# Kernel optimization log

Measured on AMD Instinct MI355X. Metric: run time of the kernel, lower is better.

Reference implementation:

```python
import jax, jax.numpy as jnp
import numpy as np

H = 256   # encoder/decoder hidden size
U = 128   # attention units


def setup_inputs() -> dict:
    key = jax.random.key(0)
    ks = jax.random.split(key, 8)
    B, Td, Te = 16, 128, 1024
    s = 1.0 / np.sqrt(H)
    return {
        "dec_outputs": jax.random.normal(ks[0], (B, Td, H), dtype=jnp.float32),
        "enc_outputs": jax.random.normal(ks[1], (B, Te, H), dtype=jnp.float32),
        "W1": jax.random.normal(ks[2], (H, U), dtype=jnp.float32) * s,
        "b1": jnp.zeros((U,), dtype=jnp.float32),
        "W2": jax.random.normal(ks[3], (H, U), dtype=jnp.float32) * s,
        "b2": jnp.zeros((U,), dtype=jnp.float32),
        "V": jax.random.normal(ks[4], (U, 1), dtype=jnp.float32) * (1.0 / np.sqrt(U)),
        "bv": jnp.zeros((1,), dtype=jnp.float32),
    }


def reference(dec_outputs, enc_outputs, W1, b1, W2, b2, V, bv):
    # Project once (the original redundantly re-projects enc_outputs per step).
    # w1d: [B, Td, U], w2e: [B, Te, U]
    w1d = jnp.einsum("bth,hu->btu", dec_outputs, W1) + b1
    w2e = jnp.einsum("bsh,hu->bsu", enc_outputs, W2) + b2
    # Additive Bahdanau score: tanh over broadcast sum -> [B, Td, Te, U]
    feat = jnp.tanh(w1d[:, :, None, :] + w2e[:, None, :, :])
    # V projection to scalar score: [B, Td, Te]
    score = jnp.einsum("btsu,u->bts", feat, V[:, 0]) + bv[0]
    # Softmax over encoder positions (original Softmax(axis=1) on [B, Te])
    return jax.nn.softmax(score, axis=-1)
```

## Files before the change

kernel.cpp:

```cpp
#include <hip/hip_runtime.h>
#include <math.h>

#define HB 256
#define UB 128
#define BB 16
#define TD 128
#define TE 1024

#define CLAMP_W 7.0f
#define L2E2 2.8853900817779268f
#define ALPHA 1.52587890625e-05f
#define NEG2ALPHA (-3.0517578125e-05f)

__device__ __forceinline__ float stage_exp(float w, float shift) {
    float t = fminf(fmaxf(w, -CLAMP_W), CLAMP_W);
    return exp2f(fmaf(t, L2E2, shift));
}

#define DEC_SLABS 32
#define NSLABS 288
#define PROJ_BLOCKS (NSLABS * 2)

__global__ __launch_bounds__(512) void proj_v12(
    const float* __restrict__ dec, const float* __restrict__ enc,
    const float* __restrict__ W1, const float* __restrict__ b1,
    const float* __restrict__ W2, const float* __restrict__ b2,
    float* __restrict__ Ea, float* __restrict__ Eb) {
    const int blk = blockIdx.x;
    const int slab = blk >> 1, uhalf = blk & 1;
    const bool is_dec = slab < DEC_SLABS;
    const int rel = is_dec ? slab : slab - DEC_SLABS;
    const float* __restrict__ X    = is_dec ? dec : enc;
    const float* __restrict__ W    = is_dec ? W1 : W2;
    const float* __restrict__ bias = is_dec ? b1 : b2;

    __shared__ float xt[HB][66];
    const int tid = threadIdx.x;
    const long row0 = (long)rel * 64;

    #pragma unroll
    for (int it = 0; it < 8; ++it) {
        int idx = it * 512 + tid;
        int row = idx >> 6, hf4 = idx & 63;
        float4 f = *reinterpret_cast<const float4*>(X + (row0 + row) * HB + hf4 * 4);
        xt[hf4 * 4 + 0][row] = f.x;
        xt[hf4 * 4 + 1][row] = f.y;
        xt[hf4 * 4 + 2][row] = f.z;
        xt[hf4 * 4 + 3][row] = f.w;
    }
    __syncthreads();

    const int l = tid & 63;
    const int w = __builtin_amdgcn_readfirstlane(tid >> 6);
    const int ub3 = w & 3;
    const int ub  = ub3 + uhalf * 4;
    const int hh  = w >> 2;
    const int u0  = ub * 16;
    const int h0  = hh * 128;

    float acc[16];
    #pragma unroll
    for (int j = 0; j < 16; ++j) acc[j] = 0.f;

    for (int h = 0; h < 128; h += 4) {
        const int hg = h0 + h;
        float4 wf[4][4];
        #pragma unroll
        for (int k = 0; k < 4; ++k)
            #pragma unroll
            for (int q = 0; q < 4; ++q)
                wf[k][q] = *reinterpret_cast<const float4*>(
                    W + (hg + k) * UB + u0 + q * 4);
        float xk[4];
        #pragma unroll
        for (int k = 0; k < 4; ++k) xk[k] = xt[hg + k][l];
        #pragma unroll
        for (int k = 0; k < 4; ++k)
            #pragma unroll
            for (int q = 0; q < 4; ++q) {
                acc[q * 4 + 0] = fmaf(xk[k], wf[k][q].x, acc[q * 4 + 0]);
                acc[q * 4 + 1] = fmaf(xk[k], wf[k][q].y, acc[q * 4 + 1]);
                acc[q * 4 + 2] = fmaf(xk[k], wf[k][q].z, acc[q * 4 + 2]);
                acc[q * 4 + 3] = fmaf(xk[k], wf[k][q].w, acc[q * 4 + 3]);
            }
    }

    __syncthreads();
    float4* red = reinterpret_cast<float4*>(&xt[0][0]);
    if (hh == 1) {
        #pragma unroll
        for (int q = 0; q < 4; ++q)
            red[((ub3 * 64 + l) << 2) + q] =
                make_float4(acc[q * 4], acc[q * 4 + 1], acc[q * 4 + 2], acc[q * 4 + 3]);
    }
    __syncthreads();
    if (hh == 0) {
        #pragma unroll
        for (int q = 0; q < 4; ++q) {
            float4 r = red[((ub3 * 64 + l) << 2) + q];
            acc[q * 4 + 0] += r.x; acc[q * 4 + 1] += r.y;
            acc[q * 4 + 2] += r.z; acc[q * 4 + 3] += r.w;
        }
        const float sh = is_dec ? -16.f : 0.f;
        const int POS  = is_dec ? TD : TE;
        const long bq  = row0 / POS;
        const int pos  = (int)(row0 % POS) + l;
        float4* dst4 = reinterpret_cast<float4*>(is_dec ? Ea : Eb);
        #pragma unroll
        for (int q = 0; q < 4; ++q) {
            float4 o = make_float4(
                stage_exp(acc[q * 4 + 0] + bias[u0 + q * 4 + 0], sh),
                stage_exp(acc[q * 4 + 1] + bias[u0 + q * 4 + 1], sh),
                stage_exp(acc[q * 4 + 2] + bias[u0 + q * 4 + 2], sh),
                stage_exp(acc[q * 4 + 3] + bias[u0 + q * 4 + 3], sh));
            dst4[(bq * 32 + ub * 4 + q) * (long)POS + pos] = o;
        }
    }
}

__global__ __launch_bounds__(512) void score_v12(
    const float4* __restrict__ Ea4,
    const float4* __restrict__ Eb4,
    const float4* __restrict__ V4,
    float* __restrict__ outraw) {
    const int tid = threadIdx.x;
    const int i = blockIdx.x;
    const int xcd = i & 7;
    const int rest = i >> 3;
    const int b = 2 * xcd + (rest >> 6);
    const int sub = rest & 63;
    const int t0 = (sub >> 3) * 16;
    const int schunk = sub & 7;

    __shared__ float4 as[512];
    __shared__ float4 vs[32];
    as[tid] = Ea4[((long)b * 32 + (tid >> 4)) * TD + t0 + (tid & 15)];
    if (tid < 32) vs[tid] = V4[tid];
    __syncthreads();

    const int l = tid & 63, wv = tid >> 6;
    const int t = l & 15, sc = l >> 4;
    const int s0 = schunk * 128 + wv * 16 + sc * 4;

    const float4* __restrict__ ep = Eb4 + (long)b * 32 * TE + s0;
    const float alphav = ALPHA;
    float acc[4] = {0.f, 0.f, 0.f, 0.f};

    #pragma unroll 2
    for (int u4 = 0; u4 < 32; ++u4) {
        float4 A  = as[u4 * 16 + t];
        float4 v4 = vs[u4];
        #pragma unroll
        for (int j = 0; j < 4; ++j) {
            float4 e = ep[(long)u4 * TE + j];
            float X0 = fmaf(A.x, e.x, alphav);
            float X1 = fmaf(A.y, e.y, alphav);
            float X2 = fmaf(A.z, e.z, alphav);
            float X3 = fmaf(A.w, e.w, alphav);
            float P01 = X0 * X1, P23 = X2 * X3;
            float N01 = fmaf(v4.x, X1, v4.y * X0);
            float N23 = fmaf(v4.z, X3, v4.w * X2);
            float N   = fmaf(N01, P23, N23 * P01);
            acc[j] = fmaf(N, __builtin_amdgcn_rcpf(P01 * P23), acc[j]);
        }
    }

    float4 o = make_float4(NEG2ALPHA * acc[0], NEG2ALPHA * acc[1],
                           NEG2ALPHA * acc[2], NEG2ALPHA * acc[3]);
    *reinterpret_cast<float4*>(&outraw[((long)b * TD + t0 + t) * TE + s0]) = o;
}

__global__ __launch_bounds__(1024) void softmax_v9(float* __restrict__ out) {
    const long row = blockIdx.x;
    float* p = out + row * TE;
    const int tid = threadIdx.x;
    const int wv = tid >> 6, l = tid & 63;

    float x = p[tid];
    __shared__ float red[16];
    float m = x;
    #pragma unroll
    for (int off = 32; off > 0; off >>= 1) m = fmaxf(m, __shfl_xor(m, off, 64));
    if (l == 0) red[wv] = m;
    __syncthreads();
    #pragma unroll
    for (int k = 0; k < 16; ++k) m = fmaxf(m, red[k]);
    __syncthreads();
    float e = __expf(x - m);
    float si = e;
    #pragma unroll
    for (int off = 32; off > 0; off >>= 1) si += __shfl_xor(si, off, 64);
    if (l == 0) red[wv] = si;
    __syncthreads();
    si = 0.f;
    #pragma unroll
    for (int k = 0; k < 16; ++k) si += red[k];
    p[tid] = e * (1.f / si);
}

extern "C" void kernel_launch(void* const* d_in, const int* in_sizes, int n_in,
                              void* d_out, int out_size, void* d_ws, size_t ws_size,
                              hipStream_t stream) {
    const float* dec = (const float*)d_in[0];
    const float* enc = (const float*)d_in[1];
    const float* W1  = (const float*)d_in[2];
    const float* b1  = (const float*)d_in[3];
    const float* W2  = (const float*)d_in[4];
    const float* b2  = (const float*)d_in[5];
    const float* V   = (const float*)d_in[6];
    float* out = (float*)d_out;

    float* Ea = (float*)d_ws;
    float* Eb = Ea + (long)BB * 32 * TD * 4;

    proj_v12<<<PROJ_BLOCKS, 512, 0, stream>>>(dec, enc, W1, b1, W2, b2, Ea, Eb);
    score_v12<<<1024, 512, 0, stream>>>(
        (const float4*)Ea, (const float4*)Eb, (const float4*)V, out);
    softmax_v9<<<BB * TD, 1024, 0, stream>>>(out);
}
```

Before: 76.83 us.

## Rework score kernel to per-thread s column with scalar-loaded decoder tiles

New measurement: 67.86 us. -11.7%, faster.

```diff
diff --git a/kernel.cpp b/kernel.cpp
--- a/kernel.cpp
+++ b/kernel.cpp
@@ -11,6 +11,11 @@
 #define L2E2 2.8853900817779268f
 #define ALPHA 1.52587890625e-05f
 #define NEG2ALPHA (-3.0517578125e-05f)
+
+#define PINV(x) asm volatile("" : "+v"(x))
+#define PINS(x) asm volatile("" : "+s"(x))
+#define PINV4(q) do { PINV((q).x); PINV((q).y); PINV((q).z); PINV((q).w); } while (0)
+#define PINS4(q) do { PINS((q).x); PINS((q).y); PINS((q).z); PINS((q).w); } while (0)
 
 __device__ __forceinline__ float stage_exp(float w, float shift) {
     float t = fminf(fmaxf(w, -CLAMP_W), CLAMP_W);
@@ -118,56 +123,63 @@
     }
 }
 
-__global__ __launch_bounds__(512) void score_v12(
-    const float4* __restrict__ Ea4,
+__global__ __launch_bounds__(512) void score_v9(
+    const float* __restrict__ Ea4,
     const float4* __restrict__ Eb4,
-    const float4* __restrict__ V4,
+    const float* __restrict__ V,
     float* __restrict__ outraw) {
     const int tid = threadIdx.x;
     const int i = blockIdx.x;
-    const int xcd = i & 7;
-    const int rest = i >> 3;
-    const int b = 2 * xcd + (rest >> 6);
-    const int sub = rest & 63;
-    const int t0 = (sub >> 3) * 16;
-    const int schunk = sub & 7;
-
-    __shared__ float4 as[512];
-    __shared__ float4 vs[32];
-    as[tid] = Ea4[((long)b * 32 + (tid >> 4)) * TD + t0 + (tid & 15)];
-    if (tid < 32) vs[tid] = V4[tid];
-    __syncthreads();
-
-    const int l = tid & 63, wv = tid >> 6;
-    const int t = l & 15, sc = l >> 4;
-    const int s0 = schunk * 128 + wv * 16 + sc * 4;
-
-    const float4* __restrict__ ep = Eb4 + (long)b * 32 * TE + s0;
+    const int xcd = i & 7, j = i >> 3;
+    const int b     = 2 * xcd + (j >> 4);
+    const int tgrp  = (j >> 1) & 7;
+    const int shalf = j & 1;
+    const int t0 = tgrp * 16;
+    const int s  = shalf * 512 + tid;
+
+    const float*  ab = Ea4 + ((long)b * 32 * TD + t0) * 4;
+    const float4* ep = Eb4 + (long)b * 32 * TE + s;
     const float alphav = ALPHA;
-    float acc[4] = {0.f, 0.f, 0.f, 0.f};
-
-    #pragma unroll 2
+
+    float acc[16];
+    #pragma unroll
+    for (int t = 0; t < 16; ++t) acc[t] = 0.f;
+
+    float4 a[16], vC, vN, eC, eN;
+    vC = *reinterpret_cast<const float4*>(V);
+    eC = ep[0];
+
     for (int u4 = 0; u4 < 32; ++u4) {
-        float4 A  = as[u4 * 16 + t];
-        float4 v4 = vs[u4];
-        #pragma unroll
-        for (int j = 0; j < 4; ++j) {
-            float4 e = ep[(long)u4 * TE + j];
-            float X0 = fmaf(A.x, e.x, alphav);
-            float X1 = fmaf(A.y, e.y, alphav);
-            float X2 = fmaf(A.z, e.z, alphav);
-            float X3 = fmaf(A.w, e.w, alphav);
+        const int p = (u4 + 1 < 32) ? u4 + 1 : 0;
+        eN = ep[(long)p * TE];
+        vN = *reinterpret_cast<const float4*>(V + p * 4);
+        const float* _a = ab + (long)u4 * (TD * 4);
+        #pragma unroll
+        for (int t = 0; t < 16; ++t)
+            a[t] = *reinterpret_cast<const float4*>(_a + t * 4);
+        PINS4(a[15]);
+        #pragma unroll
+        for (int t = 0; t < 16; ++t) {
+            float4 A = a[t];
+            float X0 = fmaf(A.x, eC.x, alphav);
+            float X1 = fmaf(A.y, eC.y, alphav);
+            float X2 = fmaf(A.z, eC.z, alphav);
+            float X3 = fmaf(A.w, eC.w, alphav);
             float P01 = X0 * X1, P23 = X2 * X3;
-            float N01 = fmaf(v4.x, X1, v4.y * X0);
-            float N23 = fmaf(v4.z, X3, v4.w * X2);
+            float N01 = fmaf(vC.x, X1, vC.y * X0);
+            float N23 = fmaf(vC.z, X3, vC.w * X2);
             float N   = fmaf(N01, P23, N23 * P01);
-            acc[j] = fmaf(N, __builtin_amdgcn_rcpf(P01 * P23), acc[j]);
+            acc[t] = fmaf(N, __builtin_amdgcn_rcpf(P01 * P23), acc[t]);
         }
-    }
-
-    float4 o = make_float4(NEG2ALPHA * acc[0], NEG2ALPHA * acc[1],
-                           NEG2ALPHA * acc[2], NEG2ALPHA * acc[3]);
-    *reinterpret_cast<float4*>(&outraw[((long)b * TD + t0 + t) * TE + s0]) = o;
+        PINV4(eN);
+        PINS4(vN);
+        eC = eN; vC = vN;
+    }
+
+    float* orow = outraw + ((long)b * TD + t0) * TE + s;
+    #pragma unroll
+    for (int t = 0; t < 16; ++t)
+        orow[(long)t * TE] = NEG2ALPHA * acc[t];
 }
 
 __global__ __launch_bounds__(1024) void softmax_v9(float* __restrict__ out) {
@@ -214,7 +226,6 @@
     float* Eb = Ea + (long)BB * 32 * TD * 4;
 
     proj_v12<<<PROJ_BLOCKS, 512, 0, stream>>>(dec, enc, W1, b1, W2, b2, Ea, Eb);
-    score_v12<<<1024, 512, 0, stream>>>(
-        (const float4*)Ea, (const float4*)Eb, (const float4*)V, out);
+    score_v9<<<256, 512, 0, stream>>>(Ea, (const float4*)Eb, V, out);
     softmax_v9<<<BB * TD, 1024, 0, stream>>>(out);
 }
```
